# Performance work log

Measured on AMD Instinct MI355X. Metric: run time of the kernel, lower is better.

The kernel has to match this reference:

```python
import jax, jax.numpy as jnp
import numpy as np

B, ENC, DEC, H, W = 8, 64, 128, 128, 128
NEG = -1e30  # masked-softmax fill


def _neighbors(x):
    """x: [B,H,W,C] -> [B,H,W,9,C] 3x3 neighborhood gather (zeros at borders)."""
    b, h, w, c = x.shape
    p = jnp.pad(x, ((0, 0), (1, 1), (1, 1), (0, 0)))
    return jnp.stack([p[:, r:r + h, c_:c_ + w, :] for r in range(3) for c_ in range(3)], axis=3)


def _neighbor_mask(h, w):
    """[H,W,9] bool: which of the 9 neighbors are in-bounds per pixel."""
    m = jnp.pad(jnp.ones((h, w), dtype=bool), ((1, 1), (1, 1)))
    return jnp.stack([m[r:r + h, c_:c_ + w] for r in range(3) for c_ in range(3)], axis=2)


def setup_inputs() -> dict:
    key = jax.random.key(0)
    ks = jax.random.split(key, 12)
    s = 0.05
    return {
        "encoder_features": jax.random.normal(ks[0], (B, ENC, H, W), jnp.float32),
        "decoder_features": jax.random.normal(ks[1], (B, DEC, H, W), jnp.float32),
        "W_enc": jax.random.normal(ks[2], (ENC, ENC), jnp.float32) * s,
        "b_enc": jax.random.normal(ks[3], (ENC,), jnp.float32) * s,
        "W_dec": jax.random.normal(ks[4], (DEC, ENC), jnp.float32) * s,
        "b_dec": jax.random.normal(ks[5], (ENC,), jnp.float32) * s,
        "W_agg": jax.random.normal(ks[6], (ENC, 1), jnp.float32) * s,
        "b_agg": jax.random.normal(ks[7], (1,), jnp.float32) * s,
        "W_attn": jax.random.normal(ks[8], (2 * ENC, ENC), jnp.float32) * s,
        "b_attn": jax.random.normal(ks[9], (ENC,), jnp.float32) * s,
        "conv_w": jax.random.normal(ks[10], (3, 3, DEC, ENC), jnp.float32) * s,  # HWIO
        "conv_b": jax.random.normal(ks[11], (ENC,), jnp.float32) * s,
    }


def reference(encoder_features, decoder_features, W_enc, b_enc, W_dec, b_dec,
              W_agg, b_agg, W_attn, b_attn, conv_w, conv_b):
    # NCHW -> NHWC (format_linear)
    enc = jnp.transpose(encoder_features, (0, 2, 3, 1))  # [B,H,W,ENC]
    dec = jnp.transpose(decoder_features, (0, 2, 3, 1))  # [B,H,W,DEC]

    q = dec @ W_dec + b_dec  # [B,H,W,ENC]
    k = enc @ W_enc + b_enc  # [B,H,W,ENC]
    vals = jax.lax.conv_general_dilated(
        dec, conv_w, window_strides=(1, 1), padding='SAME',
        dimension_numbers=('NHWC', 'HWIO', 'NHWC')) + conv_b  # [B,H,W,ENC]

    kn = _neighbors(k)    # [B,H,W,9,ENC]
    en = _neighbors(enc)  # [B,H,W,9,ENC]
    mask = _neighbor_mask(q.shape[1], q.shape[2])  # [H,W,9]

    # per-neighbor additive score: agg_encoder(tanh(query + key)) -> scalar
    scores = jnp.squeeze(jnp.tanh(q[:, :, :, None, :] + kn) @ W_agg, -1) + b_agg  # [B,H,W,9]
    scores = jnp.where(mask, scores, NEG)
    attn_w = jax.nn.softmax(scores, axis=-1)  # softmax over valid neighbors only
    attn_vec = jnp.einsum('bhwn,bhwnc->bhwc', attn_w, en)  # weighted sum of raw encoder feats

    cat = jnp.concatenate([vals, attn_vec], axis=-1)  # [B,H,W,2*ENC]
    out = cat @ W_attn + b_attn
    out = jnp.where(out >= 0, out, 0.2 * out)  # LeakyReLU(0.2)
    return jnp.transpose(out, (0, 3, 1, 2))  # back to NCHW
```

## Files before the change

kernel.cpp:

```cpp
#include <hip/hip_runtime.h>

#define BB 8
#define ENC_C 64
#define DEC_C 128
#define HH 128
#define WW 128

typedef unsigned short ushort_t;
typedef __attribute__((ext_vector_type(8))) short short8;
typedef __attribute__((ext_vector_type(4))) short short4v;
typedef __attribute__((ext_vector_type(4))) float f32x4;

static __device__ __forceinline__ ushort_t f2bf(float x) {
  unsigned int u = __builtin_bit_cast(unsigned int, x);
  u += 0x7fff + ((u >> 16) & 1);
  return (ushort_t)(u >> 16);
}
static __device__ __forceinline__ float bf2f(ushort_t v) {
  unsigned int u = ((unsigned int)v) << 16;
  return __builtin_bit_cast(float, u);
}

__global__ __launch_bounds__(64) void pack_w_kernel(
    const float* __restrict__ conv_w, const float* __restrict__ W_attn,
    const float* __restrict__ W_dec, const float* __restrict__ W_enc,
    const float* __restrict__ conv_b, const float* __restrict__ b_attn,
    ushort_t* __restrict__ packedC2, ushort_t* __restrict__ packedW2,
    ushort_t* __restrict__ packedQ, ushort_t* __restrict__ packedK,
    float* __restrict__ bias_total)
{
  const int blk = blockIdx.x;
  const int l = threadIdx.x;

  if (blk < 144) {
    const int kstep = blk >> 2, nf = blk & 3;
    const int tap = kstep >> 2, dstep = kstep & 3;
    const int n = nf * 16 + (l & 15);
    const int dbase = dstep * 32 + (l >> 4) * 8;
    float wcol[64];
    #pragma unroll
    for (int c = 0; c < 64; ++c) wcol[c] = W_attn[c * 64 + n];
    ushort_t v[8];
    #pragma unroll
    for (int j = 0; j < 8; ++j) {
      const float* cw = conv_w + ((long)(tap * DEC_C + dbase + j)) * 64;
      float acc = 0.f;
      #pragma unroll
      for (int c = 0; c < 64; ++c) acc = __builtin_fmaf(cw[c], wcol[c], acc);
      v[j] = f2bf(acc);
    }
    ushort_t* d = packedC2 + (((long)tap * 16 + dstep * 4 + nf) * 64 + l) * 8;
    #pragma unroll
    for (int j = 0; j < 8; ++j) d[j] = v[j];
    return;
  }
  if (blk == 176) {
    float acc = b_attn[l];
    #pragma unroll
    for (int c = 0; c < 64; ++c)
      acc = __builtin_fmaf(conv_b[c], W_attn[c * 64 + l], acc);
    bias_total[l] = acc;
    return;
  }

  const float* W;
  ushort_t* dst;
  int bb, krow0;
  if (blk < 152)      { W = W_attn; dst = packedW2; bb = blk - 144; krow0 = 64; }
  else if (blk < 168) { W = W_dec;  dst = packedQ;  bb = blk - 152; krow0 = 0; }
  else                { W = W_enc;  dst = packedK;  bb = blk - 168; krow0 = 0; }
  const int ks = bb >> 2, nf = bb & 3;
  const int n = nf * 16 + (l & 15);
  const int kbase = krow0 + ks * 32 + (l >> 4) * 8;
  ushort_t v[8];
  #pragma unroll
  for (int j = 0; j < 8; ++j)
    v[j] = f2bf(W[(kbase + j) * 64 + n]);
  ushort_t* d = dst + ((long)bb * 64 + l) * 8;
  #pragma unroll
  for (int j = 0; j < 8; ++j) d[j] = v[j];
}

__global__ __launch_bounds__(256) void prep_kernel(
    const float* __restrict__ enc, const float* __restrict__ dec,
    const ushort_t* __restrict__ packedQ, const ushort_t* __restrict__ packedK,
    const ushort_t* __restrict__ packedW2,
    const float* __restrict__ b_enc, const float* __restrict__ b_dec,
    ushort_t* __restrict__ q_nhwc, ushort_t* __restrict__ k_nhwc,
    ushort_t* __restrict__ encw, ushort_t* __restrict__ dec_t)
{
  __shared__ float smem[4 * 16 * 68];
  const int nwg = gridDim.x;
  const int cpx = nwg >> 3;
  const int bid = blockIdx.x;
  const int grp = (bid & 7) * cpx + (bid >> 3);
  const int b = grp >> 8;
  const int h = (grp & 255) >> 1;
  const int half = grp & 1;
  const int bh = b * HH + h;
  const int tid = threadIdx.x;
  const int l = tid & 63;
  const int wv = tid >> 6;
  const int pw = half * 64 + wv * 16;
  const int col = l & 15, kg = l >> 4;
  const long plane = (long)HH * WW;
  float* swl = smem + wv * 16 * 68;

  {
    const float* ebase = enc + ((long)(b * ENC_C) * HH + h) * WW + pw;
    #pragma unroll
    for (int i = 0; i < 16; ++i) {
      const int cc = i * 4 + kg;
      swl[col * 68 + cc] = ebase[(long)cc * plane + col];
    }

    f32x4 acck[4], accw[4];
    #pragma unroll
    for (int nf = 0; nf < 4; ++nf) {
      acck[nf] = (f32x4){0.f, 0.f, 0.f, 0.f};
      accw[nf] = (f32x4){0.f, 0.f, 0.f, 0.f};
    }

    #pragma unroll
    for (int ks = 0; ks < 2; ++ks) {
      const float4* p = (const float4*)&swl[col * 68 + ks * 32 + kg * 8];
      float4 x0 = p[0], x1 = p[1];
      short8 afr;
      afr[0] = (short)f2bf(x0.x); afr[1] = (short)f2bf(x0.y);
      afr[2] = (short)f2bf(x0.z); afr[3] = (short)f2bf(x0.w);
      afr[4] = (short)f2bf(x1.x); afr[5] = (short)f2bf(x1.y);
      afr[6] = (short)f2bf(x1.z); afr[7] = (short)f2bf(x1.w);
      #pragma unroll
      for (int nf = 0; nf < 4; ++nf) {
        const short8 bk =
            *(const short8*)(packedK + ((long)(ks * 4 + nf) * 64 + l) * 8);
        const short8 bw =
            *(const short8*)(packedW2 + ((long)(ks * 4 + nf) * 64 + l) * 8);
        acck[nf] = __builtin_amdgcn_mfma_f32_16x16x32_bf16(
            afr, bk, acck[nf], 0, 0, 0);
        accw[nf] = __builtin_amdgcn_mfma_f32_16x16x32_bf16(
            afr, bw, accw[nf], 0, 0, 0);
      }
    }
    #pragma unroll
    for (int nf = 0; nf < 4; ++nf)
      #pragma unroll
      for (int r = 0; r < 4; ++r) {
        const int px = pw + kg * 4 + r;
        const int c = nf * 16 + col;
        k_nhwc[((long)bh * WW + px) * 64 + c] = f2bf(acck[nf][r] + b_enc[c]);
        encw[((long)bh * WW + px) * 64 + c] = f2bf(accw[nf][r]);
      }
  }

  f32x4 accq[4];
  #pragma unroll
  for (int nf = 0; nf < 4; ++nf) accq[nf] = (f32x4){0.f, 0.f, 0.f, 0.f};

  #pragma unroll
  for (int hf = 0; hf < 2; ++hf) {
    const float* dbase =
        dec + ((long)(b * DEC_C + hf * 64) * HH + h) * WW + pw;
    #pragma unroll
    for (int i = 0; i < 16; ++i) {
      const int cc = i * 4 + kg;
      swl[col * 68 + cc] = dbase[(long)cc * plane + col];
    }

    #pragma unroll
    for (int i = 0; i < 4; ++i) {
      const int px = kg + i * 4;
      const float4 v = *(const float4*)&swl[px * 68 + col * 4];
      short4v s;
      s[0] = (short)f2bf(v.x); s[1] = (short)f2bf(v.y);
      s[2] = (short)f2bf(v.z); s[3] = (short)f2bf(v.w);
      *(short4v*)(dec_t + ((long)bh * WW + pw + px) * DEC_C + hf * 64 + col * 4) = s;
    }

    #pragma unroll
    for (int ks2 = 0; ks2 < 2; ++ks2) {
      const int ks = hf * 2 + ks2;
      const float4* p = (const float4*)&swl[col * 68 + ks2 * 32 + kg * 8];
      float4 x0 = p[0], x1 = p[1];
      short8 afr;
      afr[0] = (short)f2bf(x0.x); afr[1] = (short)f2bf(x0.y);
      afr[2] = (short)f2bf(x0.z); afr[3] = (short)f2bf(x0.w);
      afr[4] = (short)f2bf(x1.x); afr[5] = (short)f2bf(x1.y);
      afr[6] = (short)f2bf(x1.z); afr[7] = (short)f2bf(x1.w);
      #pragma unroll
      for (int nf = 0; nf < 4; ++nf) {
        const short8 bfr =
            *(const short8*)(packedQ + ((long)(ks * 4 + nf) * 64 + l) * 8);
        accq[nf] = __builtin_amdgcn_mfma_f32_16x16x32_bf16(
            afr, bfr, accq[nf], 0, 0, 0);
      }
    }
  }

  #pragma unroll
  for (int nf = 0; nf < 4; ++nf)
    #pragma unroll
    for (int r = 0; r < 4; ++r) {
      const int px = pw + kg * 4 + r;
      const int c = nf * 16 + col;
      q_nhwc[((long)bh * WW + px) * 64 + c] = f2bf(accq[nf][r] + b_dec[c]);
    }
}

__global__ __launch_bounds__(256) void attn_kernel(
    const ushort_t* __restrict__ q_nhwc, const ushort_t* __restrict__ k_nhwc,
    const ushort_t* __restrict__ encw, const float* __restrict__ W_agg,
    const float* __restrict__ b_agg, ushort_t* __restrict__ attw2)
{
  const int nwg = gridDim.x;
  const int cpx = nwg >> 3;
  const int bid = blockIdx.x;
  const int swz = (bid & 7) * cpx + (bid >> 3);
  const int t = swz * 256 + threadIdx.x;
  const int pix = t >> 2;
  const int cb = (t & 3) * 16;
  const int h = (pix >> 7) & 127;
  const int w = pix & 127;

  int off[9]; bool valid[9];
  #pragma unroll
  for (int n = 0; n < 9; ++n) {
    const int dh = n / 3 - 1, dw = n % 3 - 1;
    const int nh = h + dh, nw = w + dw;
    valid[n] = (nh >= 0 && nh < HH && nw >= 0 && nw < WW);
    const int nhc = min(max(nh, 0), HH - 1);
    const int nwc = min(max(nw, 0), WW - 1);
    off[n] = (pix & ~16383) + nhc * WW + nwc;
  }

  const short8* qp = (const short8*)(q_nhwc + ((long)pix << 6) + cb);
  const short8 qa = qp[0], qb = qp[1];

  float wa[16];
  {
    float4 w0 = *(const float4*)(W_agg + cb);
    float4 w1 = *(const float4*)(W_agg + cb + 4);
    float4 w2 = *(const float4*)(W_agg + cb + 8);
    float4 w3 = *(const float4*)(W_agg + cb + 12);
    wa[0]=w0.x; wa[1]=w0.y; wa[2]=w0.z; wa[3]=w0.w;
    wa[4]=w1.x; wa[5]=w1.y; wa[6]=w1.z; wa[7]=w1.w;
    wa[8]=w2.x; wa[9]=w2.y; wa[10]=w2.z; wa[11]=w2.w;
    wa[12]=w3.x; wa[13]=w3.y; wa[14]=w3.z; wa[15]=w3.w;
  }

  float s[9];
  #pragma unroll
  for (int n = 0; n < 9; ++n) {
    const short8* kp = (const short8*)(k_nhwc + ((long)off[n] << 6) + cb);
    const short8 ka = kp[0], kb = kp[1];
    float sc = 0.f;
    #pragma unroll
    for (int e = 0; e < 8; ++e) {
      float x = bf2f((ushort_t)qa[e]) + bf2f((ushort_t)ka[e]);
      x = fminf(fmaxf(x, -15.f), 15.f);
      float z = __builtin_amdgcn_exp2f(x * 2.88539008f);
      float tt = __builtin_fmaf(-2.f, __builtin_amdgcn_rcpf(z + 1.f), 1.f);
      sc = __builtin_fmaf(tt, wa[e], sc);
    }
    #pragma unroll
    for (int e = 0; e < 8; ++e) {
      float x = bf2f((ushort_t)qb[e]) + bf2f((ushort_t)kb[e]);
      x = fminf(fmaxf(x, -15.f), 15.f);
      float z = __builtin_amdgcn_exp2f(x * 2.88539008f);
      float tt = __builtin_fmaf(-2.f, __builtin_amdgcn_rcpf(z + 1.f), 1.f);
      sc = __builtin_fmaf(tt, wa[8 + e], sc);
    }
    s[n] = sc;
  }

  #pragma unroll
  for (int n = 0; n < 9; ++n) {
    s[n] += __shfl_xor(s[n], 1);
    s[n] += __shfl_xor(s[n], 2);
  }

  const float bagg = b_agg[0];
  float m = -1e30f;
  #pragma unroll
  for (int n = 0; n < 9; ++n) {
    s[n] = valid[n] ? (s[n] + bagg) : -1e30f;
    m = fmaxf(m, s[n]);
  }
  float attw[9]; float denom = 0.f;
  #pragma unroll
  for (int n = 0; n < 9; ++n) {
    attw[n] = __builtin_amdgcn_exp2f((s[n] - m) * 1.44269504f);
    denom += attw[n];
  }
  const float inv = __builtin_amdgcn_rcpf(denom);
  #pragma unroll
  for (int n = 0; n < 9; ++n) attw[n] *= inv;

  float a16[16];
  #pragma unroll
  for (int e = 0; e < 16; ++e) a16[e] = 0.f;
  #pragma unroll
  for (int n = 0; n < 9; ++n) {
    const short8* ep = (const short8*)(encw + ((long)off[n] << 6) + cb);
    const short8 ea = ep[0], eb = ep[1];
    #pragma unroll
    for (int e = 0; e < 8; ++e)
      a16[e] = __builtin_fmaf(attw[n], bf2f((ushort_t)ea[e]), a16[e]);
    #pragma unroll
    for (int e = 0; e < 8; ++e)
      a16[8 + e] = __builtin_fmaf(attw[n], bf2f((ushort_t)eb[e]), a16[8 + e]);
  }
  short8 o0, o1;
  #pragma unroll
  for (int e = 0; e < 8; ++e) {
    o0[e] = (short)f2bf(a16[e]);
    o1[e] = (short)f2bf(a16[8 + e]);
  }
  short8* op = (short8*)(attw2 + ((long)pix << 6) + cb);
  op[0] = o0;
  op[1] = o1;
}

__global__ __launch_bounds__(256) void conv2_kernel(
    const ushort_t* __restrict__ dec_t, const ushort_t* __restrict__ packedC2,
    const ushort_t* __restrict__ attw2, const float* __restrict__ bias_total,
    float* __restrict__ out)
{
  __shared__ ushort_t bsh[16384];
  const int nwg = gridDim.x;
  const int cpx = nwg >> 3;
  const int bid = blockIdx.x;
  const int bh = (bid & 7) * cpx + (bid >> 3);
  const int b = bh >> 7, h = bh & 127;
  const int tid = threadIdx.x;
  const int l = tid & 63;
  const int wv = tid >> 6;
  const int pix0 = wv * 32;
  const int col = l & 15, kg = l >> 4;

  auto stage = [&](int tap) {
    const ushort_t* src = packedC2 + (long)tap * 8192;
    ushort_t* dstb = bsh + (tap & 1) * 8192 + (long)(tid & ~63) * 8;
    #pragma unroll
    for (int i = 0; i < 4; ++i) {
      __builtin_amdgcn_global_load_lds(
          (const __attribute__((address_space(1))) void*)(src + (long)(i * 256 + tid) * 8),
          (__attribute__((address_space(3))) void*)(dstb + i * 256 * 8),
          16, 0, 0);
    }
  };

  f32x4 acc[4][2];
  #pragma unroll
  for (int mf = 0; mf < 4; ++mf)
    #pragma unroll
    for (int pf = 0; pf < 2; ++pf)
      acc[mf][pf] = (f32x4){0.f, 0.f, 0.f, 0.f};

  stage(0);

  #pragma unroll
  for (int p = 0; p < 9; ++p) {
    __syncthreads();
    if (p + 1 < 9) stage(p + 1);
    const int kh = p / 3, kw = p % 3;
    const int hh = h + kh - 1;
    if (hh >= 0 && hh < HH) {
      const ushort_t* arow = dec_t + ((long)(b * HH + hh) * WW) * DEC_C;
      const ushort_t* bbase = bsh + (p & 1) * 8192;
      short8 pfr[4][2];
      #pragma unroll
      for (int pf = 0; pf < 2; ++pf) {
        const int wp = pix0 + pf * 16 + col + kw - 1;
        const bool ok = (wp >= 0 && wp < WW);
        #pragma unroll
        for (int ds = 0; ds < 4; ++ds) {
          short8 z = {0, 0, 0, 0, 0, 0, 0, 0};
          pfr[ds][pf] = ok
              ? *(const short8*)(arow + (long)wp * DEC_C + ds * 32 + kg * 8) : z;
        }
      }
      #pragma unroll
      for (int ds = 0; ds < 4; ++ds)
        #pragma unroll
        for (int mf = 0; mf < 4; ++mf) {
          const short8 wfr =
              *(const short8*)(bbase + ((ds * 4 + mf) * 64 + l) * 8);
          acc[mf][0] = __builtin_amdgcn_mfma_f32_16x16x32_bf16(
              wfr, pfr[ds][0], acc[mf][0], 0, 0, 0);
          acc[mf][1] = __builtin_amdgcn_mfma_f32_16x16x32_bf16(
              wfr, pfr[ds][1], acc[mf][1], 0, 0, 0);
        }
    }
  }

  #pragma unroll
  for (int mf = 0; mf < 4; ++mf)
    #pragma unroll
    for (int pf = 0; pf < 2; ++pf) {
      const int pix = pix0 + pf * 16 + col;
      const short4v av = *(const short4v*)(
          attw2 + ((long)bh * WW + pix) * 64 + mf * 16 + kg * 4);
      #pragma unroll
      for (int r = 0; r < 4; ++r) {
        const int ch = mf * 16 + kg * 4 + r;
        float o = acc[mf][pf][r] + bf2f((ushort_t)av[r]) + bias_total[ch];
        o = (o >= 0.f) ? o : 0.2f * o;
        out[((long)(b * ENC_C + ch) * HH + h) * WW + pix] = o;
      }
    }
}

extern "C" void kernel_launch(void* const* d_in, const int* in_sizes, int n_in,
                              void* d_out, int out_size, void* d_ws, size_t ws_size,
                              hipStream_t stream) {
  const float* enc    = (const float*)d_in[0];
  const float* dec    = (const float*)d_in[1];
  const float* W_enc  = (const float*)d_in[2];
  const float* b_enc  = (const float*)d_in[3];
  const float* W_dec  = (const float*)d_in[4];
  const float* b_dec  = (const float*)d_in[5];
  const float* W_agg  = (const float*)d_in[6];
  const float* b_agg  = (const float*)d_in[7];
  const float* W_attn = (const float*)d_in[8];
  const float* b_attn = (const float*)d_in[9];
  const float* conv_w = (const float*)d_in[10];
  const float* conv_b = (const float*)d_in[11];
  float* out = (float*)d_out;

  const long npix = (long)BB * HH * WW;
  ushort_t* q_bf     = (ushort_t*)d_ws;
  ushort_t* k_bf     = q_bf + npix * 64;
  ushort_t* encw     = k_bf + npix * 64;
  ushort_t* dec_t    = encw + npix * 64;
  ushort_t* attw2    = dec_t + npix * 128;
  ushort_t* packedC2 = attw2 + npix * 64;
  ushort_t* packedW2 = packedC2 + 144 * 64 * 8;
  ushort_t* packedQ  = packedW2 + 8 * 64 * 8;
  ushort_t* packedK  = packedQ + 16 * 64 * 8;
  float* bias_total  = (float*)(packedK + 8 * 64 * 8);

  hipLaunchKernelGGL(pack_w_kernel, dim3(177), dim3(64), 0, stream,
                     conv_w, W_attn, W_dec, W_enc, conv_b, b_attn,
                     packedC2, packedW2, packedQ, packedK, bias_total);
  hipLaunchKernelGGL(prep_kernel, dim3(BB * HH * 2), dim3(256), 0, stream,
                     enc, dec, packedQ, packedK, packedW2, b_enc, b_dec,
                     q_bf, k_bf, encw, dec_t);
  hipLaunchKernelGGL(attn_kernel, dim3((int)(npix * 4 / 256)), dim3(256), 0, stream,
                     q_bf, k_bf, encw, W_agg, b_agg, attw2);
  hipLaunchKernelGGL(conv2_kernel, dim3(BB * HH), dim3(256), 0, stream,
                     dec_t, packedC2, attw2, bias_total, out);
}
```

Before: 120.5 us.

## Double-buffer prep tiles, vectorize global loads and repack outputs through LDS

Restructures prep_kernel to load encoder and decoder tiles with float4 global reads into two per-wave LDS buffers. The next tile's load is issued before the current tile's MFMAs so global latency overlaps compute. K, encw and Q results are staged back through LDS and written as 16-byte bf16 vectors instead of scattered 2-byte stores, and the dec_t stores are widened the same way. The kernel also gains a min-blocks-per-CU hint of 2. LDS usage doubles and there are extra LDS round trips, with no explicit barriers since each wave uses only its own buffers.

```diff
diff --git a/kernel.cpp b/kernel.cpp
--- a/kernel.cpp
+++ b/kernel.cpp
@@ -81,7 +81,7 @@
   for (int j = 0; j < 8; ++j) d[j] = v[j];
 }
 
-__global__ __launch_bounds__(256) void prep_kernel(
+__global__ __launch_bounds__(256, 2) void prep_kernel(
     const float* __restrict__ enc, const float* __restrict__ dec,
     const ushort_t* __restrict__ packedQ, const ushort_t* __restrict__ packedK,
     const ushort_t* __restrict__ packedW2,
@@ -89,7 +89,7 @@
     ushort_t* __restrict__ q_nhwc, ushort_t* __restrict__ k_nhwc,
     ushort_t* __restrict__ encw, ushort_t* __restrict__ dec_t)
 {
-  __shared__ float smem[4 * 16 * 68];
+  __shared__ float smem[4 * 2 * 16 * 68];
   const int nwg = gridDim.x;
   const int cpx = nwg >> 3;
   const int bid = blockIdx.x;
@@ -103,108 +103,126 @@
   const int wv = tid >> 6;
   const int pw = half * 64 + wv * 16;
   const int col = l & 15, kg = l >> 4;
+  const int a4 = l & 3, c16 = l >> 2;
   const long plane = (long)HH * WW;
-  float* swl = smem + wv * 16 * 68;
-
-  {
-    const float* ebase = enc + ((long)(b * ENC_C) * HH + h) * WW + pw;
-    #pragma unroll
-    for (int i = 0; i < 16; ++i) {
-      const int cc = i * 4 + kg;
-      swl[col * 68 + cc] = ebase[(long)cc * plane + col];
-    }
-
-    f32x4 acck[4], accw[4];
+  float* bufA = smem + wv * 2 * 1088;
+  float* bufB = bufA + 1088;
+
+  auto load_tile = [&](const float* base, float* buf) {
+    #pragma unroll
+    for (int it = 0; it < 4; ++it) {
+      const int p = it * 16 + c16;
+      const float4 v = *(const float4*)(base + (long)p * plane + a4 * 4);
+      buf[(a4 * 4 + 0) * 68 + p] = v.x;
+      buf[(a4 * 4 + 1) * 68 + p] = v.y;
+      buf[(a4 * 4 + 2) * 68 + p] = v.z;
+      buf[(a4 * 4 + 3) * 68 + p] = v.w;
+    }
+  };
+  auto make_frag = [&](const float* buf, int koff) -> short8 {
+    const float4 x0 = *(const float4*)&buf[col * 68 + koff];
+    const float4 x1 = *(const float4*)&buf[col * 68 + koff + 4];
+    short8 v;
+    v[0] = (short)f2bf(x0.x); v[1] = (short)f2bf(x0.y);
+    v[2] = (short)f2bf(x0.z); v[3] = (short)f2bf(x0.w);
+    v[4] = (short)f2bf(x1.x); v[5] = (short)f2bf(x1.y);
+    v[6] = (short)f2bf(x1.z); v[7] = (short)f2bf(x1.w);
+    return v;
+  };
+  auto repack_store = [&](const f32x4* acc, const float* bias, ushort_t* dst,
+                          float* buf) {
     #pragma unroll
     for (int nf = 0; nf < 4; ++nf) {
-      acck[nf] = (f32x4){0.f, 0.f, 0.f, 0.f};
-      accw[nf] = (f32x4){0.f, 0.f, 0.f, 0.f};
-    }
-
-    #pragma unroll
-    for (int ks = 0; ks < 2; ++ks) {
-      const float4* p = (const float4*)&swl[col * 68 + ks * 32 + kg * 8];
-      float4 x0 = p[0], x1 = p[1];
-      short8 afr;
-      afr[0] = (short)f2bf(x0.x); afr[1] = (short)f2bf(x0.y);
-      afr[2] = (short)f2bf(x0.z); afr[3] = (short)f2bf(x0.w);
-      afr[4] = (short)f2bf(x1.x); afr[5] = (short)f2bf(x1.y);
-      afr[6] = (short)f2bf(x1.z); afr[7] = (short)f2bf(x1.w);
+      const float bb = bias ? bias[nf * 16 + col] : 0.f;
       #pragma unroll
-      for (int nf = 0; nf < 4; ++nf) {
-        const short8 bk =
-            *(const short8*)(packedK + ((long)(ks * 4 + nf) * 64 + l) * 8);
-        const short8 bw =
-            *(const short8*)(packedW2 + ((long)(ks * 4 + nf) * 64 + l) * 8);
-        acck[nf] = __builtin_amdgcn_mfma_f32_16x16x32_bf16(
-            afr, bk, acck[nf], 0, 0, 0);
-        accw[nf] = __builtin_amdgcn_mfma_f32_16x16x32_bf16(
-            afr, bw, accw[nf], 0, 0, 0);
-      }
-    }
-    #pragma unroll
-    for (int nf = 0; nf < 4; ++nf)
-      #pragma unroll
-      for (int r = 0; r < 4; ++r) {
-        const int px = pw + kg * 4 + r;
-        const int c = nf * 16 + col;
-        k_nhwc[((long)bh * WW + px) * 64 + c] = f2bf(acck[nf][r] + b_enc[c]);
-        encw[((long)bh * WW + px) * 64 + c] = f2bf(accw[nf][r]);
-      }
-  }
-
-  f32x4 accq[4];
-  #pragma unroll
-  for (int nf = 0; nf < 4; ++nf) accq[nf] = (f32x4){0.f, 0.f, 0.f, 0.f};
-
-  #pragma unroll
-  for (int hf = 0; hf < 2; ++hf) {
-    const float* dbase =
-        dec + ((long)(b * DEC_C + hf * 64) * HH + h) * WW + pw;
-    #pragma unroll
-    for (int i = 0; i < 16; ++i) {
-      const int cc = i * 4 + kg;
-      swl[col * 68 + cc] = dbase[(long)cc * plane + col];
-    }
-
-    #pragma unroll
-    for (int i = 0; i < 4; ++i) {
-      const int px = kg + i * 4;
-      const float4 v = *(const float4*)&swl[px * 68 + col * 4];
-      short4v s;
-      s[0] = (short)f2bf(v.x); s[1] = (short)f2bf(v.y);
-      s[2] = (short)f2bf(v.z); s[3] = (short)f2bf(v.w);
-      *(short4v*)(dec_t + ((long)bh * WW + pw + px) * DEC_C + hf * 64 + col * 4) = s;
-    }
-
-    #pragma unroll
-    for (int ks2 = 0; ks2 < 2; ++ks2) {
-      const int ks = hf * 2 + ks2;
-      const float4* p = (const float4*)&swl[col * 68 + ks2 * 32 + kg * 8];
-      float4 x0 = p[0], x1 = p[1];
-      short8 afr;
-      afr[0] = (short)f2bf(x0.x); afr[1] = (short)f2bf(x0.y);
-      afr[2] = (short)f2bf(x0.z); afr[3] = (short)f2bf(x0.w);
-      afr[4] = (short)f2bf(x1.x); afr[5] = (short)f2bf(x1.y);
-      afr[6] = (short)f2bf(x1.z); afr[7] = (short)f2bf(x1.w);
-      #pragma unroll
-      for (int nf = 0; nf < 4; ++nf) {
-        const short8 bfr =
-            *(const short8*)(packedQ + ((long)(ks * 4 + nf) * 64 + l) * 8);
-        accq[nf] = __builtin_amdgcn_mfma_f32_16x16x32_bf16(
-            afr, bfr, accq[nf], 0, 0, 0);
-      }
-    }
-  }
-
-  #pragma unroll
-  for (int nf = 0; nf < 4; ++nf)
-    #pragma unroll
-    for (int r = 0; r < 4; ++r) {
-      const int px = pw + kg * 4 + r;
-      const int c = nf * 16 + col;
-      q_nhwc[((long)bh * WW + px) * 64 + c] = f2bf(accq[nf][r] + b_dec[c]);
-    }
+      for (int r = 0; r < 4; ++r)
+        buf[(kg * 4 + r) * 68 + nf * 16 + col] = acc[nf][r] + bb;
+    }
+    #pragma unroll
+    for (int j = 0; j < 2; ++j) {
+      const int px = c16;
+      const int c8 = (a4 + 4 * j) * 8;
+      const float4 x0 = *(const float4*)&buf[px * 68 + c8];
+      const float4 x1 = *(const float4*)&buf[px * 68 + c8 + 4];
+      short8 s;
+      s[0] = (short)f2bf(x0.x); s[1] = (short)f2bf(x0.y);
+      s[2] = (short)f2bf(x0.z); s[3] = (short)f2bf(x0.w);
+      s[4] = (short)f2bf(x1.x); s[5] = (short)f2bf(x1.y);
+      s[6] = (short)f2bf(x1.z); s[7] = (short)f2bf(x1.w);
+      *(short8*)(dst + (((long)(bh * WW + pw + px)) << 6) + c8) = s;
+    }
+  };
+  auto dect_store = [&](const float* buf, int hf) {
+    #pragma unroll
+    for (int j = 0; j < 2; ++j) {
+      const int px = c16;
+      const int c8 = (a4 + 4 * j) * 8;
+      const float4 x0 = *(const float4*)&buf[px * 68 + c8];
+      const float4 x1 = *(const float4*)&buf[px * 68 + c8 + 4];
+      short8 s;
+      s[0] = (short)f2bf(x0.x); s[1] = (short)f2bf(x0.y);
+      s[2] = (short)f2bf(x0.z); s[3] = (short)f2bf(x0.w);
+      s[4] = (short)f2bf(x1.x); s[5] = (short)f2bf(x1.y);
+      s[6] = (short)f2bf(x1.z); s[7] = (short)f2bf(x1.w);
+      *(short8*)(dec_t + (((long)(bh * WW + pw + px)) << 7) + hf * 64 + c8) = s;
+    }
+  };
+
+  f32x4 acck[4], accw[4], accq[4];
+  #pragma unroll
+  for (int nf = 0; nf < 4; ++nf) {
+    acck[nf] = (f32x4){0.f, 0.f, 0.f, 0.f};
+    accw[nf] = (f32x4){0.f, 0.f, 0.f, 0.f};
+    accq[nf] = (f32x4){0.f, 0.f, 0.f, 0.f};
+  }
+
+  load_tile(enc + ((long)(b * ENC_C) * HH + h) * WW + pw, bufA);
+  load_tile(dec + ((long)(b * DEC_C) * HH + h) * WW + pw, bufB);
+
+  #pragma unroll
+  for (int ks = 0; ks < 2; ++ks) {
+    const short8 afr = make_frag(bufA, ks * 32 + kg * 8);
+    #pragma unroll
+    for (int nf = 0; nf < 4; ++nf) {
+      const short8 bk =
+          *(const short8*)(packedK + ((long)(ks * 4 + nf) * 64 + l) * 8);
+      const short8 bw =
+          *(const short8*)(packedW2 + ((long)(ks * 4 + nf) * 64 + l) * 8);
+      acck[nf] = __builtin_amdgcn_mfma_f32_16x16x32_bf16(afr, bk, acck[nf], 0, 0, 0);
+      accw[nf] = __builtin_amdgcn_mfma_f32_16x16x32_bf16(afr, bw, accw[nf], 0, 0, 0);
+    }
+  }
+
+  load_tile(dec + ((long)(b * DEC_C + 64) * HH + h) * WW + pw, bufA);
+
+  #pragma unroll
+  for (int ks2 = 0; ks2 < 2; ++ks2) {
+    const short8 afr = make_frag(bufB, ks2 * 32 + kg * 8);
+    #pragma unroll
+    for (int nf = 0; nf < 4; ++nf) {
+      const short8 bq =
+          *(const short8*)(packedQ + ((long)(ks2 * 4 + nf) * 64 + l) * 8);
+      accq[nf] = __builtin_amdgcn_mfma_f32_16x16x32_bf16(afr, bq, accq[nf], 0, 0, 0);
+    }
+  }
+  dect_store(bufB, 0);
+
+  repack_store(acck, b_enc, k_nhwc, bufB);
+  repack_store(accw, nullptr, encw, bufB);
+
+  #pragma unroll
+  for (int ks2 = 0; ks2 < 2; ++ks2) {
+    const short8 afr = make_frag(bufA, ks2 * 32 + kg * 8);
+    #pragma unroll
+    for (int nf = 0; nf < 4; ++nf) {
+      const short8 bq =
+          *(const short8*)(packedQ + ((long)((2 + ks2) * 4 + nf) * 64 + l) * 8);
+      accq[nf] = __builtin_amdgcn_mfma_f32_16x16x32_bf16(afr, bq, accq[nf], 0, 0, 0);
+    }
+  }
+  dect_store(bufA, 1);
+
+  repack_store(accq, b_dec, q_nhwc, bufA);
 }
 
 __global__ __launch_bounds__(256) void attn_kernel(
```

New measurement: 120.9 us (median of 2 runs). Within noise of the previous version (+0.3%).
